# Optimization experiments

Measured on AMD Instinct MI355X. Metric: run time of the kernel, lower is better.

Reference implementation:

```python
import jax, jax.numpy as jnp
import numpy as np

L, B, D, N = 2048, 8, 1024, 64

def setup_inputs() -> dict:
    key = jax.random.key(0)
    ks = jax.random.split(key, 6)
    return {
        "x": jax.random.normal(ks[0], (L, B, D), dtype=jnp.float32),
        "damping_factor": jax.random.normal(ks[1], (D, N, 1), dtype=jnp.float32),
        "decay_factor": jax.random.normal(ks[2], (D, N, 1), dtype=jnp.float32),
        "ema_expansion_matrix": jax.random.normal(ks[3], (D, N, 1), dtype=jnp.float32),
        "kernel_projection_matrix": jax.random.normal(ks[4], (D, N), dtype=jnp.float32),
        "residual_weight": jax.random.normal(ks[5], (D,), dtype=jnp.float32),
    }

def reference(x, damping_factor, decay_factor, ema_expansion_matrix,
              kernel_projection_matrix, residual_weight):
    seq_len, bsz, dim = x.shape
    ndim = damping_factor.shape[1]
    # --- kernel synthesis (training path, unidirectional) ---
    damping = jax.nn.sigmoid(damping_factor)           # (D, N, 1)
    decay = jax.nn.sigmoid(decay_factor)               # (D, N, 1)
    prev_w = 1.0 - damping * decay                     # (D, N, 1), in (0,1)
    t = jnp.arange(seq_len, dtype=jnp.float32)[None, None, :]  # (1,1,L)
    vander = t * jnp.log(prev_w)                       # (D, N, L)
    kernel_vals = damping * ema_expansion_matrix * jnp.exp(vander)  # (D,N,L)
    kernel = jnp.einsum('dnl,dn->dl', kernel_vals, kernel_projection_matrix)
    kernel = kernel * np.float32(1.0 / np.sqrt(ndim))  # (D, L)
    # --- residual + FFT long convolution ---
    residual = x * residual_weight                     # (L, B, D)
    x_conv = jnp.transpose(x, (1, 2, 0))               # (B, D, L)
    n_fft = 2 * seq_len
    x_fft = jnp.fft.rfft(x_conv, n=n_fft)              # (B, D, n/2+1)
    k_fft = jnp.fft.rfft(kernel, n=n_fft)              # (D, n/2+1)
    conv = jnp.fft.irfft(x_fft * k_fft, n=n_fft)[..., :seq_len]  # (B, D, L)
    ema_out = jnp.transpose(conv, (2, 0, 1))           # (L, B, D)
    return jax.nn.silu(ema_out + residual)
```

## Files before the change

kernel.cpp:

```cpp
#include <hip/hip_runtime.h>
#include <hip/hip_bf16.h>


#define BSZ 8
#define DIM 1024
#define ND 64
#define BD 8192
#define SEGS 4
#define SEGLEN 512
#define CH1 64
#define CPS1 8
#define TD 16
#define XP1 68
#define NCH2 16
#define YP2 17

typedef short bf16x8 __attribute__((ext_vector_type(8)));
typedef float f32x4 __attribute__((ext_vector_type(4)));
union BF8 { uint32_t u[4]; bf16x8 v; };
#define MFMA __builtin_amdgcn_mfma_f32_16x16x32_bf16

__device__ __forceinline__ uint32_t pk_bf16(float a, float b) {
    __hip_bfloat162 h2 = __float22bfloat162_rn(make_float2(a, b));
    uint32_t u; __builtin_memcpy(&u, &h2, 4);
    return u;
}

__device__ __forceinline__ void block_sync_lds() {
    asm volatile("s_waitcnt lgkmcnt(0)" ::: "memory");
    __builtin_amdgcn_s_barrier();
    asm volatile("" ::: "memory");
}

__global__ __launch_bounds__(128, 8) void mega_pass1(
    const float* __restrict__ x,
    const float* __restrict__ dfp,
    const float* __restrict__ cfp,
    ushort* __restrict__ S)
{
    __shared__ float xb[2][TD * XP1];

    const int tid = threadIdx.x;
    const int lane = tid & 63;
    const int wv = tid >> 6;
    const int q   = (lane & 3) | (((lane >> 3) & 1) << 2);
    const int col = wv * 8 + ((lane >> 2) & 1) + ((lane >> 4) & 3) * 2;
    const int blk = blockIdx.x;
    const int dt  = blk & 63;
    const int b   = (blk >> 6) & 7;
    const int seg = blk >> 9;
    const int d   = dt * TD + col;

    float w[8];
    {
        const int pb = d * ND + q * 8;
        const float4 df0 = *(const float4*)(dfp + pb);
        const float4 df1 = *(const float4*)(dfp + pb + 4);
        const float4 cf0 = *(const float4*)(cfp + pb);
        const float4 cf1 = *(const float4*)(cfp + pb + 4);
        const float dfv[8] = {df0.x, df0.y, df0.z, df0.w, df1.x, df1.y, df1.z, df1.w};
        const float cfv[8] = {cf0.x, cf0.y, cf0.z, cf0.w, cf1.x, cf1.y, cf1.z, cf1.w};
        #pragma unroll
        for (int i = 0; i < 8; ++i) {
            const float sd = 1.0f / (1.0f + __expf(-dfv[i]));
            const float sc = 1.0f / (1.0f + __expf(-cfv[i]));
            w[i] = 1.0f - sd * sc;
        }
    }

    const int r0 = tid >> 2;
    const int c4 = (tid & 3) * 4;
    const float* xg = x + (size_t)(seg * SEGLEN) * BD + b * DIM + dt * TD;

    float4 nx0 = *(const float4*)(xg + (size_t)r0 * BD + c4);
    float4 nx1 = *(const float4*)(xg + (size_t)(r0 + 32) * BD + c4);

    float h[8];
    #pragma unroll
    for (int i = 0; i < 8; ++i) h[i] = 0.0f;

    for (int g = 0; g < CPS1; ++g) {
        float* xbuf = xb[g & 1];
        const float nv0[4] = {nx0.x, nx0.y, nx0.z, nx0.w};
        const float nv1[4] = {nx1.x, nx1.y, nx1.z, nx1.w};
        #pragma unroll
        for (int e = 0; e < 4; ++e) {
            xbuf[(c4 + e) * XP1 + r0]      = nv0[e];
            xbuf[(c4 + e) * XP1 + r0 + 32] = nv1[e];
        }
        if (g + 1 < CPS1) {
            nx0 = *(const float4*)(xg + (size_t)((g + 1) * CH1 + r0) * BD + c4);
            nx1 = *(const float4*)(xg + (size_t)((g + 1) * CH1 + r0 + 32) * BD + c4);
        }
        block_sync_lds();

        const float* xcol = xbuf + col * XP1;
        #pragma unroll 2
        for (int t8 = 0; t8 < 8; ++t8) {
            const float4 tva = *(const float4*)(xcol + t8 * 8);
            const float4 tvb = *(const float4*)(xcol + t8 * 8 + 4);
            const float tvs[8] = {tva.x, tva.y, tva.z, tva.w,
                                  tvb.x, tvb.y, tvb.z, tvb.w};
            #pragma unroll
            for (int k = 0; k < 8; ++k) {
                const float xv = tvs[k];
                #pragma unroll
                for (int i = 0; i < 8; ++i) h[i] = fmaf(w[i], h[i], xv);
            }
        }
    }

    const size_t sb = ((size_t)(seg * BSZ + b) * 64 + dt) * 1024 + col * 64 + q * 8;
    uint32_t pk[4] = {pk_bf16(h[0], h[1]), pk_bf16(h[2], h[3]),
                      pk_bf16(h[4], h[5]), pk_bf16(h[6], h[7])};
    *(uint4*)(S + sb) = make_uint4(pk[0], pk[1], pk[2], pk[3]);
}

__global__ __launch_bounds__(1024, 4) void mega_pass2(
    const float* __restrict__ x,
    const float* __restrict__ dfp,
    const float* __restrict__ cfp,
    const float* __restrict__ emp,
    const float* __restrict__ pjp,
    const float* __restrict__ rwp,
    const ushort* __restrict__ S,
    float* __restrict__ out)
{
    __shared__ __align__(16) float    xb[2][TD * 8 * 36];
    __shared__ __align__(16) float    yt[2][256 * YP2];
    __shared__ __align__(16) uint32_t hbq[16 * 256];
    __shared__ __align__(8)  float2   pclw[16 * 64];
    __shared__ float kap[16 * 32];

    const int tid = threadIdx.x;
    const int tl  = tid & 63;
    const int wv  = tid >> 6;
    const int c   = tl & 15;
    const int g   = tl >> 4;
    const int cq  = c & 7;
    const int hf  = c >> 3;
    const int blk = blockIdx.x;
    const int seg = blk >> 6;
    const int dt  = blk & 63;
    const int d0  = dt * TD;
    const int d   = d0 + wv;

    {
        const int pidx = d * ND + tl;
        const float sd = 1.0f / (1.0f + __expf(-dfp[pidx]));
        const float sc = 1.0f / (1.0f + __expf(-cfp[pidx]));
        const float wn = 1.0f - sd * sc;
        const float cn = sd * emp[pidx] * pjp[pidx] * 0.125f;
        pclw[wv * 64 + tl] = make_float2(cn, log2f(wn));
    }
    const float rwd = rwp[d];

    const int drow = tid & 15;
    const int bq   = (tid >> 4) & 7;
    const int l4g  = tid >> 7;
    const int gsw  = 4 * (l4g ^ (drow & 6));
    const int xwoff = (drow * 8 + bq) * 36 + gsw;
    const float* xgs = x + (size_t)(seg * SEGLEN + 4 * l4g) * BD + bq * DIM + d0 + drow;
    float nx0 = xgs[0];
    float nx1 = xgs[(size_t)BD];
    float nx2 = xgs[(size_t)2 * BD];
    float nx3 = xgs[(size_t)3 * BD];

    const int rid = tid >> 2;
    const int l_s = rid >> 3;
    const int b_s = rid & 7;
    const int dq  = tid & 3;
    const int yrho = b_s + 8 * ((l_s >> 2) & 3) + 32 * (l_s & 3) + 128 * (l_s >> 4);

    float lw16[16];
    #pragma unroll
    for (int T = 0; T < 4; ++T)
        #pragma unroll
        for (int r = 0; r < 4; ++r)
            lw16[T * 4 + r] = pclw[wv * 64 + 16 * T + 4 * g + r].y;

    float h[16];
    #pragma unroll
    for (int i = 0; i < 16; ++i) h[i] = 0.0f;
    if (seg > 0) {
        float w512[16];
        #pragma unroll
        for (int i = 0; i < 16; ++i) w512[i] = exp2f(512.0f * lw16[i]);
        for (int sp = 0; sp < seg; ++sp) {
            const size_t sbase = ((size_t)(sp * BSZ + cq) * 64 + dt) * 1024 + wv * 64;
            #pragma unroll
            for (int T = 0; T < 4; ++T) {
                const uint2 u = *(const uint2*)(S + sbase + 16 * T + 4 * g);
                const float s0 = __uint_as_float(u.x << 16);
                const float s1 = __uint_as_float(u.x & 0xFFFF0000u);
                const float s2 = __uint_as_float(u.y << 16);
                const float s3 = __uint_as_float(u.y & 0xFFFF0000u);
                h[T*4+0] = fmaf(w512[T*4+0], h[T*4+0], s0);
                h[T*4+1] = fmaf(w512[T*4+1], h[T*4+1], s1);
                h[T*4+2] = fmaf(w512[T*4+2], h[T*4+2], s2);
                h[T*4+3] = fmaf(w512[T*4+3], h[T*4+3], s3);
            }
        }
    }
    float w32[16];
    #pragma unroll
    for (int i = 0; i < 16; ++i) w32[i] = exp2f(32.0f * lw16[i]);

    BF8 Vf[4], T2f[2][2], Kf[2];
    #pragma unroll
    for (int T = 0; T < 4; ++T) {
        const float2 pcl = pclw[wv * 64 + 16 * T + c];
        const float winv = exp2f(-pcl.y);
        float ve = exp2f((float)(31 - 8 * g) * pcl.y);
        float vv[8];
        #pragma unroll
        for (int e = 0; e < 8; ++e) { vv[e] = ve; ve *= winv; }
        #pragma unroll
        for (int j = 0; j < 4; ++j) Vf[T].u[j] = pk_bf16(vv[2*j], vv[2*j+1]);
    }
    #pragma unroll
    for (int Tk = 0; Tk < 2; ++Tk) {
        float2 m8[8];
        #pragma unroll
        for (int e = 0; e < 8; ++e) m8[e] = pclw[wv * 64 + 32 * Tk + 8 * g + e];
        #pragma unroll
        for (int Tj = 0; Tj < 2; ++Tj) {
            const float jf = (float)(16 * Tj + c + 1);
            float tv[8];
            #pragma unroll
            for (int e = 0; e < 8; ++e) tv[e] = m8[e].x * exp2f(jf * m8[e].y);
            #pragma unroll
            for (int j = 0; j < 4; ++j) T2f[Tj][Tk].u[j] = pk_bf16(tv[2*j], tv[2*j+1]);
        }
    }
    {
        const int p = tl >> 1, half = tl & 1;
        float acc = 0.0f;
        for (int i = 0; i < 32; ++i) {
            const float2 pc = pclw[wv * 64 + half * 32 + i];
            acc = fmaf(pc.x, exp2f((float)p * pc.y), acc);
        }
        const int prt = __builtin_amdgcn_update_dpp(0, __float_as_int(acc), 0xB1, 0xF, 0xF, true);
        acc += __int_as_float(prt);
        if (!half) kap[wv * 32 + p] = acc;
    }
    #pragma unroll
    for (int Tj = 0; Tj < 2; ++Tj) {
        float kv[8];
        #pragma unroll
        for (int e = 0; e < 8; ++e) {
            const int pp = 16 * Tj + c - 8 * g - e;
            float kv_;
            if (pp > 0)       kv_ = kap[wv * 32 + pp];
            else if (pp == 0) kv_ = kap[wv * 32] + rwd;
            else              kv_ = 0.0f;
            kv[e] = kv_;
        }
        #pragma unroll
        for (int j = 0; j < 4; ++j) Kf[Tj].u[j] = pk_bf16(kv[2*j], kv[2*j+1]);
    }

    const int sgm = wv & 6;
    const int kb  = 4 * ((2 * g) ^ sgm);
    const int swzc = ((c & 3) << 3) | (((c >> 2) & 1) << 2);
    uint32_t* hbw = hbq + wv * 256 + cq * 32;
    float* ogbase = out + (size_t)(seg * SEGLEN) * BD + d0;
    const f32x4 zf = {0.0f, 0.0f, 0.0f, 0.0f};

    if (hf == 0) {
        #pragma unroll
        for (int T = 0; T < 4; ++T) {
            const int p0 = 8 * T + 2 * g;
            *(uint2*)(&hbw[p0 ^ swzc]) =
                make_uint2(pk_bf16(h[4*T+0], h[4*T+1]), pk_bf16(h[4*T+2], h[4*T+3]));
        }
    }
    BF8 hB0, hB1;
    {
        const uint4 a  = *(const uint4*)(&hbw[(4 * g) ^ swzc]);
        const uint4 b2 = *(const uint4*)(&hbw[(16 + 4 * g) ^ swzc]);
        hB0.u[0]=a.x;  hB0.u[1]=a.y;  hB0.u[2]=a.z;  hB0.u[3]=a.w;
        hB1.u[0]=b2.x; hB1.u[1]=b2.y; hB1.u[2]=b2.z; hB1.u[3]=b2.w;
    }
    {
        *(float4*)(&xb[0][xwoff]) = make_float4(nx0, nx1, nx2, nx3);
        const float* xp = xgs + (size_t)32 * BD;
        nx0 = xp[0]; nx1 = xp[(size_t)BD]; nx2 = xp[(size_t)2*BD]; nx3 = xp[(size_t)3*BD];
    }
    block_sync_lds();

    for (int ch = 0; ch < NCH2; ++ch) {
        const float* xrow = xb[ch & 1] + (wv * 8 + cq) * 36;

        BF8 xB;
        {
            const float4 fa = *(const float4*)(xrow + kb);
            const float4 fb = *(const float4*)(xrow + kb + 4);
            xB.u[0] = pk_bf16(fa.x, fa.y); xB.u[1] = pk_bf16(fa.z, fa.w);
            xB.u[2] = pk_bf16(fb.x, fb.y); xB.u[3] = pk_bf16(fb.z, fb.w);
        }

        if (ch + 1 < NCH2) {
            *(float4*)(&xb[(ch + 1) & 1][xwoff]) = make_float4(nx0, nx1, nx2, nx3);
            if (ch + 2 < NCH2) {
                const float* xp = xgs + (size_t)(ch + 2) * 32 * BD;
                nx0 = xp[0]; nx1 = xp[(size_t)BD]; nx2 = xp[(size_t)2*BD]; nx3 = xp[(size_t)3*BD];
            }
        }
        if (ch > 0) {
            const float* yprev = yt[(ch - 1) & 1];
            float ov[4];
            #pragma unroll
            for (int e = 0; e < 4; ++e) ov[e] = yprev[yrho * YP2 + 4 * dq + e];
            *(float4*)(ogbase + (size_t)((ch - 1) * 32 + l_s) * BD + b_s * DIM + 4 * dq) =
                make_float4(ov[0], ov[1], ov[2], ov[3]);
        }

        f32x4 y0 = MFMA(Kf[0].v, xB.v, zf, 0, 0, 0);
        f32x4 y1 = MFMA(Kf[1].v, xB.v, zf, 0, 0, 0);
        y0 = MFMA(T2f[0][0].v, hB0.v, y0, 0, 0, 0);
        y1 = MFMA(T2f[1][0].v, hB0.v, y1, 0, 0, 0);
        y0 = MFMA(T2f[0][1].v, hB1.v, y0, 0, 0, 0);
        y1 = MFMA(T2f[1][1].v, hB1.v, y1, 0, 0, 0);
        #pragma unroll
        for (int T = 0; T < 4; ++T) {
            const f32x4 U = MFMA(Vf[T].v, xB.v, zf, 0, 0, 0);
            h[4*T+0] = fmaf(w32[4*T+0], h[4*T+0], U[0]);
            h[4*T+1] = fmaf(w32[4*T+1], h[4*T+1], U[1]);
            h[4*T+2] = fmaf(w32[4*T+2], h[4*T+2], U[2]);
            h[4*T+3] = fmaf(w32[4*T+3], h[4*T+3], U[3]);
        }
        if (hf == 0) {
            #pragma unroll
            for (int T = 0; T < 4; ++T) {
                const int p0 = 8 * T + 2 * g;
                *(uint2*)(&hbw[p0 ^ swzc]) =
                    make_uint2(pk_bf16(h[4*T+0], h[4*T+1]), pk_bf16(h[4*T+2], h[4*T+3]));
            }
        }
        {
            const uint4 a  = *(const uint4*)(&hbw[(4 * g) ^ swzc]);
            const uint4 b2 = *(const uint4*)(&hbw[(16 + 4 * g) ^ swzc]);
            hB0.u[0]=a.x;  hB0.u[1]=a.y;  hB0.u[2]=a.z;  hB0.u[3]=a.w;
            hB1.u[0]=b2.x; hB1.u[1]=b2.y; hB1.u[2]=b2.z; hB1.u[3]=b2.w;
        }

        {
            float* ycur = yt[ch & 1];
            const f32x4 yy = hf ? y1 : y0;
            #pragma unroll
            for (int r = 0; r < 4; ++r) {
                const float v = yy[r];
                const float sv = v / (1.0f + __expf(-v));
                ycur[(cq + 8 * (g + 4 * r + 16 * hf)) * YP2 + wv] = sv;
            }
        }
        block_sync_lds();
    }

    {
        const float* yprev = yt[(NCH2 - 1) & 1];
        float ov[4];
        #pragma unroll
        for (int e = 0; e < 4; ++e) ov[e] = yprev[yrho * YP2 + 4 * dq + e];
        *(float4*)(ogbase + (size_t)((NCH2 - 1) * 32 + l_s) * BD + b_s * DIM + 4 * dq) =
            make_float4(ov[0], ov[1], ov[2], ov[3]);
    }
}

extern "C" void kernel_launch(void* const* d_in, const int* in_sizes, int n_in,
                              void* d_out, int out_size, void* d_ws, size_t ws_size,
                              hipStream_t stream) {
    const float* x  = (const float*)d_in[0];
    const float* df = (const float*)d_in[1];
    const float* cf = (const float*)d_in[2];
    const float* em = (const float*)d_in[3];
    const float* pj = (const float*)d_in[4];
    const float* rw = (const float*)d_in[5];
    float* out = (float*)d_out;
    ushort* S  = (ushort*)d_ws;

    mega_pass1<<<dim3((SEGS - 1) * BSZ * 64), dim3(128), 0, stream>>>(x, df, cf, S);
    mega_pass2<<<dim3(SEGS * 64), dim3(1024), 0, stream>>>(x, df, cf, em, pj, rw, S, out);
}
```

Baseline: 74.68 us.

## Stage x tile in LDS as bf16 and remap thread-to-data indexing

```diff
diff --git a/kernel.cpp b/kernel.cpp
--- a/kernel.cpp
+++ b/kernel.cpp
@@ -126,7 +126,7 @@
     const ushort* __restrict__ S,
     float* __restrict__ out)
 {
-    __shared__ __align__(16) float    xb[2][TD * 8 * 36];
+    __shared__ __align__(16) ushort   xbh[2][TD * 8 * 32];
     __shared__ __align__(16) float    yt[2][256 * YP2];
     __shared__ __align__(16) uint32_t hbq[16 * 256];
     __shared__ __align__(8)  float2   pclw[16 * 64];
@@ -156,21 +156,24 @@
     const float rwd = rwp[d];
 
     const int drow = tid & 15;
-    const int bq   = (tid >> 4) & 7;
-    const int l4g  = tid >> 7;
-    const int gsw  = 4 * (l4g ^ (drow & 6));
-    const int xwoff = (drow * 8 + bq) * 36 + gsw;
+    const int bq   = ((tid >> 4) & 1) | (((tid >> 6) & 1) << 1) | (((tid >> 8) & 1) << 2);
+    const int l4g  = ((tid >> 5) & 1) | (((tid >> 7) & 1) << 1) | (((tid >> 9) & 1) << 2);
+    const int Gst  = l4g >> 1;
+    const int Hst  = l4g & 1;
+    const int Kst  = ((bq >> 1) & 3) ^ (drow & 3);
+    const int xwoff = (drow * 8 + bq) * 32 + ((Gst ^ Kst) << 3) + Hst * 4;
     const float* xgs = x + (size_t)(seg * SEGLEN + 4 * l4g) * BD + bq * DIM + d0 + drow;
     float nx0 = xgs[0];
     float nx1 = xgs[(size_t)BD];
     float nx2 = xgs[(size_t)2 * BD];
     float nx3 = xgs[(size_t)3 * BD];
 
-    const int rid = tid >> 2;
-    const int l_s = rid >> 3;
-    const int b_s = rid & 7;
     const int dq  = tid & 3;
-    const int yrho = b_s + 8 * ((l_s >> 2) & 3) + 32 * (l_s & 3) + 128 * (l_s >> 4);
+    const int b_s = (tid >> 2) & 7;
+    const int u_s = (tid >> 5) & 7;
+    const int r_s = tid >> 8;
+    const int yrow = b_s + 8 * u_s + 64 * r_s;
+    const int lam  = 4 * u_s + r_s;
 
     float lw16[16];
     #pragma unroll
@@ -260,8 +263,8 @@
         for (int j = 0; j < 4; ++j) Kf[Tj].u[j] = pk_bf16(kv[2*j], kv[2*j+1]);
     }
 
-    const int sgm = wv & 6;
-    const int kb  = 4 * ((2 * g) ^ sgm);
+    const int Krd   = ((cq >> 1) & 3) ^ (wv & 3);
+    const int xroff = (wv * 8 + cq) * 32 + ((g ^ Krd) << 3);
     const int swzc = ((c & 3) << 3) | (((c >> 2) & 1) << 2);
     uint32_t* hbw = hbq + wv * 256 + cq * 32;
     float* ogbase = out + (size_t)(seg * SEGLEN) * BD + d0;
@@ -283,25 +286,19 @@
         hB1.u[0]=b2.x; hB1.u[1]=b2.y; hB1.u[2]=b2.z; hB1.u[3]=b2.w;
     }
     {
-        *(float4*)(&xb[0][xwoff]) = make_float4(nx0, nx1, nx2, nx3);
+        *(uint2*)(&xbh[0][xwoff]) = make_uint2(pk_bf16(nx0, nx1), pk_bf16(nx2, nx3));
         const float* xp = xgs + (size_t)32 * BD;
         nx0 = xp[0]; nx1 = xp[(size_t)BD]; nx2 = xp[(size_t)2*BD]; nx3 = xp[(size_t)3*BD];
     }
     block_sync_lds();
 
     for (int ch = 0; ch < NCH2; ++ch) {
-        const float* xrow = xb[ch & 1] + (wv * 8 + cq) * 36;
-
         BF8 xB;
-        {
-            const float4 fa = *(const float4*)(xrow + kb);
-            const float4 fb = *(const float4*)(xrow + kb + 4);
-            xB.u[0] = pk_bf16(fa.x, fa.y); xB.u[1] = pk_bf16(fa.z, fa.w);
-            xB.u[2] = pk_bf16(fb.x, fb.y); xB.u[3] = pk_bf16(fb.z, fb.w);
-        }
+        xB.v = *(const bf16x8*)(&xbh[ch & 1][xroff]);
 
         if (ch + 1 < NCH2) {
-            *(float4*)(&xb[(ch + 1) & 1][xwoff]) = make_float4(nx0, nx1, nx2, nx3);
+            *(uint2*)(&xbh[(ch + 1) & 1][xwoff]) =
+                make_uint2(pk_bf16(nx0, nx1), pk_bf16(nx2, nx3));
             if (ch + 2 < NCH2) {
                 const float* xp = xgs + (size_t)(ch + 2) * 32 * BD;
                 nx0 = xp[0]; nx1 = xp[(size_t)BD]; nx2 = xp[(size_t)2*BD]; nx3 = xp[(size_t)3*BD];
@@ -311,8 +308,8 @@
             const float* yprev = yt[(ch - 1) & 1];
             float ov[4];
             #pragma unroll
-            for (int e = 0; e < 4; ++e) ov[e] = yprev[yrho * YP2 + 4 * dq + e];
-            *(float4*)(ogbase + (size_t)((ch - 1) * 32 + l_s) * BD + b_s * DIM + 4 * dq) =
+            for (int e = 0; e < 4; ++e) ov[e] = yprev[yrow * YP2 + 4 * dq + e];
+            *(float4*)(ogbase + (size_t)((ch - 1) * 32 + lam) * BD + b_s * DIM + 4 * dq) =
                 make_float4(ov[0], ov[1], ov[2], ov[3]);
         }
 
@@ -352,7 +349,7 @@
             for (int r = 0; r < 4; ++r) {
                 const float v = yy[r];
                 const float sv = v / (1.0f + __expf(-v));
-                ycur[(cq + 8 * (g + 4 * r + 16 * hf)) * YP2 + wv] = sv;
+                ycur[(cq + 8 * g + 32 * hf + 64 * r) * YP2 + wv] = sv;
             }
         }
         block_sync_lds();
@@ -362,8 +359,8 @@
         const float* yprev = yt[(NCH2 - 1) & 1];
         float ov[4];
         #pragma unroll
-        for (int e = 0; e < 4; ++e) ov[e] = yprev[yrho * YP2 + 4 * dq + e];
-        *(float4*)(ogbase + (size_t)((NCH2 - 1) * 32 + l_s) * BD + b_s * DIM + 4 * dq) =
+        for (int e = 0; e < 4; ++e) ov[e] = yprev[yrow * YP2 + 4 * dq + e];
+        *(float4*)(ogbase + (size_t)((NCH2 - 1) * 32 + lam) * BD + b_s * DIM + 4 * dq) =
             make_float4(ov[0], ov[1], ov[2], ov[3]);
     }
 }
```

Result: no change. 75.99 us (+1.8%).
